# Kernel optimization log

Hardware: AMD Instinct MI355X
Metric: run time of the kernel (lower is better)

The kernel has to match this reference:

```python
import jax, jax.numpy as jnp
import numpy as np

N, E = 50000, 800000
IN, HID, HEADS, OUT = 128, 32, 4, 64
NEG_SLOPE = 0.2
BN_EPS = 1e-5


def setup_inputs() -> dict:
    key = jax.random.key(0)
    ks = jax.random.split(key, 24)
    d1 = HID * HEADS  # 128
    def glorot(k, shape):
        fan = shape[0] + shape[-1]
        return jax.random.uniform(k, shape, jnp.float32, -1.0, 1.0) * jnp.sqrt(6.0 / fan)
    inp = {
        'x': jax.random.normal(ks[0], (N, IN), jnp.float32),
        'edge_index': jax.random.randint(ks[1], (2, E), 0, N, jnp.int64),
        # layer 1: in -> hid x heads
        'W1': glorot(ks[2], (IN, d1)),
        'as1': glorot(ks[3], (HEADS, HID)),
        'ad1': glorot(ks[4], (HEADS, HID)),
        'b1': jnp.zeros((d1,), jnp.float32),
        'g1': jnp.ones((d1,), jnp.float32),
        'be1': jnp.zeros((d1,), jnp.float32),
        # layer 2: d1 -> hid x heads
        'W2': glorot(ks[5], (d1, d1)),
        'as2': glorot(ks[6], (HEADS, HID)),
        'ad2': glorot(ks[7], (HEADS, HID)),
        'b2': jnp.zeros((d1,), jnp.float32),
        'g2': jnp.ones((d1,), jnp.float32),
        'be2': jnp.zeros((d1,), jnp.float32),
        # layer 3: d1 -> out, heads=1, concat=False
        'W3': glorot(ks[8], (d1, OUT)),
        'as3': glorot(ks[9], (1, OUT)),
        'ad3': glorot(ks[10], (1, OUT)),
        'b3': jnp.zeros((OUT,), jnp.float32),
        'g3': jnp.ones((OUT,), jnp.float32),
        'be3': jnp.zeros((OUT,), jnp.float32),
    }
    return inp


def gat_conv(x, src, dst, W, a_s, a_d, b, heads, ch, concat):
    n = x.shape[0]
    h = (x @ W).reshape(n, heads, ch)                       # [N,H,C]
    al_s = jnp.sum(h * a_s, axis=-1)                        # [N,H]
    al_d = jnp.sum(h * a_d, axis=-1)                        # [N,H]
    e = jax.nn.leaky_relu(al_s[src] + al_d[dst], NEG_SLOPE)  # [E,H]
    m = jax.ops.segment_max(e, dst, num_segments=n)
    m = jnp.where(jnp.isfinite(m), m, 0.0)
    ex = jnp.exp(e - m[dst])
    denom = jax.ops.segment_sum(ex, dst, num_segments=n)
    alpha = ex / (denom[dst] + 1e-16)                       # segment softmax
    out = jax.ops.segment_sum(h[src] * alpha[:, :, None], dst, num_segments=n)
    out = out.reshape(n, heads * ch) if concat else out.mean(axis=1)
    return out + b


def batch_norm(x, g, b):
    mu = x.mean(axis=0)
    var = x.var(axis=0)
    return (x - mu) * jax.lax.rsqrt(var + BN_EPS) * g + b


def reference(x, edge_index, W1, as1, ad1, b1, g1, be1,
              W2, as2, ad2, b2, g2, be2,
              W3, as3, ad3, b3, g3, be3):
    n = x.shape[0]
    loops = jnp.arange(n, dtype=edge_index.dtype)
    src = jnp.concatenate([edge_index[0], loops])  # add_self_loops=True
    dst = jnp.concatenate([edge_index[1], loops])
    h = gat_conv(x, src, dst, W1, as1, ad1, b1, HEADS, HID, True)
    h = jax.nn.elu(batch_norm(h, g1, be1))
    h = gat_conv(h, src, dst, W2, as2, ad2, b2, HEADS, HID, True)
    h = jax.nn.elu(batch_norm(h, g2, be2))
    h = gat_conv(h, src, dst, W3, as3, ad3, b3, 1, OUT, False)
    h = jax.nn.elu(batch_norm(h, g3, be3))
    return h
```

## Files before the change

kernel.cpp:

```cpp
#include <hip/hip_runtime.h>
#include <hip/hip_bf16.h>
#include <math.h>

#define NEG_SLOPE 0.2f
#define BN_EPS 1e-5f

using short8_t = __attribute__((ext_vector_type(8))) short;
using f32x4    = __attribute__((ext_vector_type(4))) float;

__device__ __forceinline__ unsigned short f2bf(float f) {
    unsigned int u = __float_as_uint(f);
    u += 0x7FFF + ((u >> 16) & 1);
    return (unsigned short)(u >> 16);
}
__device__ __forceinline__ float bf2f(unsigned short h) {
    return __uint_as_float(((unsigned int)h) << 16);
}

__global__ void fill_i32(int* p, int v, long long n) {
    long long i = (long long)blockIdx.x * blockDim.x + threadIdx.x;
    long long st = (long long)gridDim.x * blockDim.x;
    for (; i < n; i += st) p[i] = v;
}


__global__ void dst_count(const int* __restrict__ ei, int E, int N,
                          int* __restrict__ count, int* __restrict__ ord)
{
    long long total = (long long)E + N;
    long long st = (long long)gridDim.x * blockDim.x;
    for (long long e = (long long)blockIdx.x * blockDim.x + threadIdx.x; e < total; e += st) {
        int dt = (e < E) ? ei[E + e] : (int)(e - E);
        ord[e] = atomicAdd(&count[dt], 1);
    }
}

__global__ void block_sum(const int* __restrict__ count, int* __restrict__ bsum, int N)
{
    __shared__ int sh[256];
    int b = blockIdx.x, t = threadIdx.x;
    int base = b * 1024;
    int s = 0;
    for (int i = t; i < 1024; i += 256) {
        int j = base + i;
        if (j < N) s += count[j];
    }
    sh[t] = s;
    __syncthreads();
    for (int off = 128; off > 0; off >>= 1) {
        if (t < off) sh[t] += sh[t + off];
        __syncthreads();
    }
    if (t == 0) bsum[b] = sh[0];
}

__global__ void scan_bsum(int* __restrict__ bsum, int nb, int* __restrict__ rowptr, int N, int total)
{
    __shared__ int sh[256];
    int t = threadIdx.x;
    sh[t] = (t < nb) ? bsum[t] : 0;
    __syncthreads();
    for (int off = 1; off < 256; off <<= 1) {
        int u = (t >= off) ? sh[t - off] : 0;
        __syncthreads();
        sh[t] += u;
        __syncthreads();
    }
    if (t < nb) bsum[t] = (t == 0) ? 0 : sh[t - 1];
    if (t == 0) rowptr[N] = total;
}

__global__ void scan_final(const int* __restrict__ count, const int* __restrict__ boff,
                           int* __restrict__ rowptr, int N)
{
    __shared__ int sh[256];
    int b = blockIdx.x, t = threadIdx.x;
    int base = b * 1024 + t * 4;
    int c[4];
    int s = 0;
    #pragma unroll
    for (int i = 0; i < 4; ++i) {
        int j = base + i;
        c[i] = (j < N) ? count[j] : 0;
        s += c[i];
    }
    sh[t] = s;
    __syncthreads();
    for (int off = 1; off < 256; off <<= 1) {
        int u = (t >= off) ? sh[t - off] : 0;
        __syncthreads();
        sh[t] += u;
        __syncthreads();
    }
    int run = boff[b] + ((t == 0) ? 0 : sh[t - 1]);
    #pragma unroll
    for (int i = 0; i < 4; ++i) {
        int j = base + i;
        if (j < N) rowptr[j] = run;
        run += c[i];
    }
}

__global__ void csr_scatter(const int* __restrict__ ei, int E, int N,
                            const int* __restrict__ rowptr, const int* __restrict__ ord,
                            int* __restrict__ srcs)
{
    long long total = (long long)E + N;
    long long st = (long long)gridDim.x * blockDim.x;
    for (long long e = (long long)blockIdx.x * blockDim.x + threadIdx.x; e < total; e += st) {
        int s, dt;
        if (e < E) { s = ei[e]; dt = ei[E + e]; }
        else       { s = dt = (int)(e - E); }
        srcs[rowptr[dt] + ord[e]] = s;
    }
}


template<int D>
__global__ void prep_wfrag(const float* __restrict__ W, unsigned short* __restrict__ Wf)
{
    constexpr int CS = D / 32;
    int idx = blockIdx.x * 256 + threadIdx.x;
    if (idx >= 128 * D) return;
    int i    = idx & 7;
    int lane = (idx >> 3) & 63;
    int f    = idx >> 9;
    int ks   = f & 3;
    int cs   = (f >> 2) % CS;
    int wc   = (f >> 2) / CS;
    int k = ks * 32 + ((lane >> 4) << 3) + i;
    int d = wc * (D / 2) + cs * 16 + (lane & 15);
    Wf[idx] = f2bf(W[k * D + d]);
}

template<int D, bool BN>
__global__ __launch_bounds__(256, 4) void gemm_mfma(
        const float* __restrict__ x, const unsigned short* __restrict__ Wf,
        const float* __restrict__ colstats, const float* __restrict__ g,
        const float* __restrict__ be, unsigned short* __restrict__ hbuf,
        int N, float invN)
{
    constexpr int CS = D / 32;
    __shared__ unsigned short xs[32 * 136];
    __shared__ float affA[128], affB[128];
    int tid = threadIdx.x, lane = tid & 63, w = tid >> 6;
    int wr = w >> 1, wc = w & 1;
    int n0 = blockIdx.x * 32;

    short8_t bfr[CS][4];
    #pragma unroll
    for (int cs = 0; cs < CS; ++cs)
        #pragma unroll
        for (int ks = 0; ks < 4; ++ks)
            bfr[cs][ks] = *(const short8_t*)(Wf + (((wc * CS + cs) * 4 + ks) << 9) + (lane << 3));

    if (BN) {
        if (tid < 128) {
            float cs_ = colstats[tid], cq = colstats[tid + 128];
            float mu = cs_ * invN;
            float var = cq * invN - mu * mu;
            float s = rsqrtf(var + BN_EPS) * g[tid];
            affA[tid] = s;
            affB[tid] = be[tid] - mu * s;
        }
        __syncthreads();
    }

    for (int jj = tid; jj < 32 * 32; jj += 256) {
        int r = jj >> 5, q = jj & 31;
        float4 v = make_float4(0.f, 0.f, 0.f, 0.f);
        if (n0 + r < N) v = *(const float4*)(x + (long long)(n0 + r) * 128 + q * 4);
        if (BN) {
            int c = q * 4;
            v.x = affA[c]     * v.x + affB[c];
            v.y = affA[c + 1] * v.y + affB[c + 1];
            v.z = affA[c + 2] * v.z + affB[c + 2];
            v.w = affA[c + 3] * v.w + affB[c + 3];
            v.x = (v.x > 0.f) ? v.x : expm1f(v.x);
            v.y = (v.y > 0.f) ? v.y : expm1f(v.y);
            v.z = (v.z > 0.f) ? v.z : expm1f(v.z);
            v.w = (v.w > 0.f) ? v.w : expm1f(v.w);
        }
        ushort4 o;
        o.x = f2bf(v.x); o.y = f2bf(v.y); o.z = f2bf(v.z); o.w = f2bf(v.w);
        *(ushort4*)(xs + r * 136 + q * 4) = o;
    }
    __syncthreads();

    f32x4 acc[CS];
    #pragma unroll
    for (int cs = 0; cs < CS; ++cs) acc[cs] = (f32x4){0.f, 0.f, 0.f, 0.f};

    #pragma unroll
    for (int ks = 0; ks < 4; ++ks) {
        short8_t a = *(const short8_t*)(xs + (wr * 16 + (lane & 15)) * 136
                                           + ks * 32 + ((lane >> 4) << 3));
        #pragma unroll
        for (int cs = 0; cs < CS; ++cs)
            acc[cs] = __builtin_amdgcn_mfma_f32_16x16x32_bf16(a, bfr[cs][ks], acc[cs], 0, 0, 0);
    }

    int mrow = wr * 16 + ((lane >> 4) << 2);
    int dcol = wc * (D / 2) + (lane & 15);
    #pragma unroll
    for (int cs = 0; cs < CS; ++cs)
        #pragma unroll
        for (int r = 0; r < 4; ++r) {
            int n = n0 + mrow + r;
            if (n < N) hbuf[(long long)n * D + dcol + cs * 16] = f2bf(acc[cs][r]);
        }
}

template<int H, int C>
__global__ void calc_al(const unsigned short* __restrict__ hbuf,
                        const float* __restrict__ a_s, const float* __restrict__ a_d,
                        float* __restrict__ als, float* __restrict__ ald, int N)
{
    int idx = blockIdx.x * blockDim.x + threadIdx.x;
    if (idx >= N * H) return;
    int n = idx / H, hh = idx % H;
    const unsigned short* hp = hbuf + (long long)n * H * C + hh * C;
    float s1 = 0.f, s2 = 0.f;
    #pragma unroll
    for (int c = 0; c < C; c += 4) {
        ushort4 hv = *(const ushort4*)(hp + c);
        float f0 = bf2f(hv.x), f1 = bf2f(hv.y), f2 = bf2f(hv.z), f3 = bf2f(hv.w);
        s1 += f0 * a_s[hh * C + c]     + f1 * a_s[hh * C + c + 1]
            + f2 * a_s[hh * C + c + 2] + f3 * a_s[hh * C + c + 3];
        s2 += f0 * a_d[hh * C + c]     + f1 * a_d[hh * C + c + 1]
            + f2 * a_d[hh * C + c + 2] + f3 * a_d[hh * C + c + 3];
    }
    als[idx] = s1;
    ald[idx] = s2;
}

template<int H, int C>
__global__ __launch_bounds__(256) void gat_aggregate_v5(
        const int* __restrict__ rowptr, const int* __restrict__ srcs,
        const float* __restrict__ als, const float* __restrict__ ald,
        const unsigned short* __restrict__ hbuf, float* __restrict__ agg,
        float* __restrict__ part, int N)
{
    constexpr int D = H * C;
    constexpr int TPN = D / 8;
    constexpr int NPB = 256 / TPN;
    __shared__ float red[4][TPN * 16];
    int tid = threadIdx.x;
    int g = tid / TPN, l = tid % TPN;
    int n = blockIdx.x * NPB + g;
    bool active = (n < N);
    int c0 = l * 8;
    int hh = c0 / C;
    float aldv = active ? ald[(long long)n * H + hh] : 0.f;
    int beg = 0, end = 0;
    if (active) { beg = rowptr[n]; end = rowptr[n + 1]; }

    float wsum = 0.f;
    float acc[8];
    #pragma unroll
    for (int i = 0; i < 8; ++i) acc[i] = 0.f;

    int e = beg;
    for (; e + 4 <= end; e += 4) {
        int s0 = srcs[e], s1 = srcs[e + 1], s2 = srcs[e + 2], s3 = srcs[e + 3];
        float v0 = als[(long long)s0 * H + hh] + aldv;
        float v1 = als[(long long)s1 * H + hh] + aldv;
        float v2 = als[(long long)s2 * H + hh] + aldv;
        float v3 = als[(long long)s3 * H + hh] + aldv;
        v0 = (v0 >= 0.f) ? v0 : NEG_SLOPE * v0;
        v1 = (v1 >= 0.f) ? v1 : NEG_SLOPE * v1;
        v2 = (v2 >= 0.f) ? v2 : NEG_SLOPE * v2;
        v3 = (v3 >= 0.f) ? v3 : NEG_SLOPE * v3;
        float w0 = __expf(v0), w1 = __expf(v1), w2 = __expf(v2), w3 = __expf(v3);
        float4 q0 = *(const float4*)(hbuf + (long long)s0 * D + c0);
        float4 q1 = *(const float4*)(hbuf + (long long)s1 * D + c0);
        float4 q2 = *(const float4*)(hbuf + (long long)s2 * D + c0);
        float4 q3 = *(const float4*)(hbuf + (long long)s3 * D + c0);
        wsum += w0 + w1 + w2 + w3;
        const float* qf0 = (const float*)&q0;
        const float* qf1 = (const float*)&q1;
        const float* qf2 = (const float*)&q2;
        const float* qf3 = (const float*)&q3;
        #pragma unroll
        for (int i = 0; i < 4; ++i) {
            unsigned int u0 = __float_as_uint(qf0[i]);
            unsigned int u1 = __float_as_uint(qf1[i]);
            unsigned int u2 = __float_as_uint(qf2[i]);
            unsigned int u3 = __float_as_uint(qf3[i]);
            acc[2*i]   += w0 * __uint_as_float(u0 << 16)
                        + w1 * __uint_as_float(u1 << 16)
                        + w2 * __uint_as_float(u2 << 16)
                        + w3 * __uint_as_float(u3 << 16);
            acc[2*i+1] += w0 * __uint_as_float(u0 & 0xFFFF0000u)
                        + w1 * __uint_as_float(u1 & 0xFFFF0000u)
                        + w2 * __uint_as_float(u2 & 0xFFFF0000u)
                        + w3 * __uint_as_float(u3 & 0xFFFF0000u);
        }
    }
    for (; e < end; ++e) {
        int s = srcs[e];
        float v = als[(long long)s * H + hh] + aldv;
        v = (v >= 0.f) ? v : NEG_SLOPE * v;
        float w = __expf(v);
        float4 q = *(const float4*)(hbuf + (long long)s * D + c0);
        const float* qf = (const float*)&q;
        wsum += w;
        #pragma unroll
        for (int i = 0; i < 4; ++i) {
            unsigned int u = __float_as_uint(qf[i]);
            acc[2*i]   += w * __uint_as_float(u << 16);
            acc[2*i+1] += w * __uint_as_float(u & 0xFFFF0000u);
        }
    }
    float inv = active ? 1.f / (wsum + 1e-16f) : 0.f;
    float sv[16];
    #pragma unroll
    for (int i = 0; i < 8; ++i) {
        float o = acc[i] * inv;
        sv[i] = o;
        sv[8 + i] = o * o;
        acc[i] = o;
    }
    if (active) {
        *(float4*)(agg + (long long)n * D + c0)     = make_float4(acc[0], acc[1], acc[2], acc[3]);
        *(float4*)(agg + (long long)n * D + c0 + 4) = make_float4(acc[4], acc[5], acc[6], acc[7]);
    }

    #pragma unroll
    for (int off = TPN; off < 64; off <<= 1)
        #pragma unroll
        for (int j = 0; j < 16; ++j)
            sv[j] += __shfl_xor(sv[j], off);

    int w4 = tid >> 6, lane = tid & 63;
    if (lane < TPN) {
        #pragma unroll
        for (int j = 0; j < 16; ++j) red[w4][lane * 16 + j] = sv[j];
    }
    __syncthreads();
    if (w4 == 0 && lane < TPN) {
        #pragma unroll
        for (int ww = 1; ww < 4; ++ww)
            #pragma unroll
            for (int j = 0; j < 16; ++j) sv[j] += red[ww][lane * 16 + j];
        float* p = part + (long long)blockIdx.x * (2 * D) + lane * 16;
        *(float4*)(p)      = make_float4(sv[0],  sv[1],  sv[2],  sv[3]);
        *(float4*)(p + 4)  = make_float4(sv[4],  sv[5],  sv[6],  sv[7]);
        *(float4*)(p + 8)  = make_float4(sv[8],  sv[9],  sv[10], sv[11]);
        *(float4*)(p + 12) = make_float4(sv[12], sv[13], sv[14], sv[15]);
    }
}

template<int D>
__global__ __launch_bounds__(256) void reduce_stats(
        const float* __restrict__ part, int nblk, float* __restrict__ colsum)
{
    __shared__ float sh[256];
    int f = blockIdx.x;
    int t = threadIdx.x;
    int col = (f < D) ? f : (f - D);
    int off = (col / 8) * 16 + (col % 8) + ((f < D) ? 0 : 8);
    float s = 0.f;
    for (int i = t; i < nblk; i += 256)
        s += part[(long long)i * (2 * D) + off];
    sh[t] = s;
    __syncthreads();
    for (int o = 128; o > 0; o >>= 1) {
        if (t < o) sh[t] += sh[t + o];
        __syncthreads();
    }
    if (t == 0) colsum[(f < D) ? f : (128 + f - D)] = sh[0];
}

template<int D>
__global__ __launch_bounds__(256) void bn_apply_v2(
        const float* __restrict__ agg, const float* __restrict__ colsum,
        const float* __restrict__ g, const float* __restrict__ be,
        float* __restrict__ out, int N, float invN)
{
    constexpr int TPR = D / 4;
    constexpr int RPB = 256 / TPR;
    __shared__ float affA[D], affB[D];
    int tid = threadIdx.x;
    if (tid < D) {
        float mu = colsum[tid] * invN;
        float var = colsum[128 + tid] * invN - mu * mu;
        float s = rsqrtf(var + BN_EPS) * g[tid];
        affA[tid] = s;
        affB[tid] = be[tid] - mu * s;
    }
    __syncthreads();
    int rg = tid / TPR, cl = tid % TPR;
    int c = cl * 4;
    float a0 = affA[c], a1 = affA[c+1], a2 = affA[c+2], a3 = affA[c+3];
    float b0 = affB[c], b1 = affB[c+1], b2 = affB[c+2], b3 = affB[c+3];
    for (int r = blockIdx.x * RPB + rg; r < N; r += gridDim.x * RPB) {
        float4 v = *(const float4*)(agg + (long long)r * D + c);
        v.x = a0 * v.x + b0; v.y = a1 * v.y + b1;
        v.z = a2 * v.z + b2; v.w = a3 * v.w + b3;
        v.x = (v.x > 0.f) ? v.x : expm1f(v.x);
        v.y = (v.y > 0.f) ? v.y : expm1f(v.y);
        v.z = (v.z > 0.f) ? v.z : expm1f(v.z);
        v.w = (v.w > 0.f) ? v.w : expm1f(v.w);
        *(float4*)(out + (long long)r * D + c) = v;
    }
}

template<int H, int C, bool BN>
static void run_layer(const float* xin, int N,
                      const int* rowptr, const int* srcs,
                      const unsigned short* Wf, const float* a_s, const float* a_d,
                      const float* prev_stats, const float* prev_g, const float* prev_be,
                      unsigned short* hbuf, float* als, float* ald,
                      float* part, float* stats_out, float* agg,
                      hipStream_t stream)
{
    constexpr int D = H * C;
    constexpr int NPB = 256 / (D / 8);
    int nblk = (N + NPB - 1) / NPB;
    float invN = 1.f / (float)N;
    gemm_mfma<D, BN><<<(N + 31) / 32, 256, 0, stream>>>(
        xin, Wf, prev_stats, prev_g, prev_be, hbuf, N, invN);
    calc_al<H, C><<<(N * H + 255) / 256, 256, 0, stream>>>(hbuf, a_s, a_d, als, ald, N);
    gat_aggregate_v5<H, C><<<nblk, 256, 0, stream>>>(
        rowptr, srcs, als, ald, hbuf, agg, part, N);
    reduce_stats<D><<<2 * D, 256, 0, stream>>>(part, nblk, stats_out);
}

extern "C" void kernel_launch(void* const* d_in, const int* in_sizes, int n_in,
                              void* d_out, int out_size, void* d_ws, size_t ws_size,
                              hipStream_t stream)
{
    const float* x   = (const float*)d_in[0];
    const int*   ei  = (const int*)d_in[1];
    const float* W1  = (const float*)d_in[2];
    const float* as1 = (const float*)d_in[3];
    const float* ad1 = (const float*)d_in[4];
    const float* g1  = (const float*)d_in[6];
    const float* be1 = (const float*)d_in[7];
    const float* W2  = (const float*)d_in[8];
    const float* as2 = (const float*)d_in[9];
    const float* ad2 = (const float*)d_in[10];
    const float* g2  = (const float*)d_in[12];
    const float* be2 = (const float*)d_in[13];
    const float* W3  = (const float*)d_in[14];
    const float* as3 = (const float*)d_in[15];
    const float* ad3 = (const float*)d_in[16];
    const float* g3  = (const float*)d_in[18];
    const float* be3 = (const float*)d_in[19];

    const int N = in_sizes[0] / 128;
    const int E = in_sizes[1] / 2;
    const int NB = (N + 1023) / 1024;
    const int NBLK128 = (N + 15) / 16;

    float* ws   = (float*)d_ws;
    float* aggA = ws;
    float* aggB = aggA + (long long)N * 128;
    float* als  = aggB + (long long)N * 128;
    float* ald  = als  + (long long)N * 4;
    float* cs0  = ald  + (long long)N * 4;
    float* cs1  = cs0 + 256;
    float* cs2  = cs1 + 256;
    unsigned short* hbuf = (unsigned short*)(cs2 + 256);
    int*   rowptr = (int*)(hbuf + (long long)N * 128);
    int*   count  = rowptr + (N + 1);
    int*   bsum   = count + N;
    int*   ord    = bsum + 256;
    int*   srcs   = ord + ((long long)E + N);
    unsigned short* wf1 = (unsigned short*)(srcs + ((long long)E + N));
    unsigned short* wf2 = wf1 + 128 * 128;
    unsigned short* wf3 = wf2 + 128 * 128;
    float* part = (float*)(wf3 + 128 * 64);

    prep_wfrag<128><<<64, 256, 0, stream>>>(W1, wf1);
    prep_wfrag<128><<<64, 256, 0, stream>>>(W2, wf2);
    prep_wfrag<64><<<32, 256, 0, stream>>>(W3, wf3);

    fill_i32<<<128, 256, 0, stream>>>(count, 0, N);
    dst_count<<<2048, 256, 0, stream>>>(ei, E, N, count, ord);
    block_sum<<<NB, 256, 0, stream>>>(count, bsum, N);
    scan_bsum<<<1, 256, 0, stream>>>(bsum, NB, rowptr, N, E + N);
    scan_final<<<NB, 256, 0, stream>>>(count, bsum, rowptr, N);
    csr_scatter<<<2048, 256, 0, stream>>>(ei, E, N, rowptr, ord, srcs);

    run_layer<4, 32, false>(x, N, rowptr, srcs, wf1, as1, ad1,
                            nullptr, nullptr, nullptr,
                            hbuf, als, ald, part, cs0, aggA, stream);
    run_layer<4, 32, true>(aggA, N, rowptr, srcs, wf2, as2, ad2,
                           cs0, g1, be1,
                           hbuf, als, ald, part, cs1, aggB, stream);
    run_layer<1, 64, true>(aggB, N, rowptr, srcs, wf3, as3, ad3,
                           cs1, g2, be2,
                           hbuf, als, ald, part, cs2, aggA, stream);
    bn_apply_v2<64><<<2048, 256, 0, stream>>>(aggA, cs2, g3, be3, (float*)d_out, N, 1.f / (float)N);
}
```

Before: 247.6 us.

## Fuse attention logit computation into GEMM epilogue and merge setup kernels

Computes the per-node source and destination attention scores inside the MFMA GEMM epilogue, using register accumulators, lane shuffles and a small shared-memory reduction for the single-head layer. This removes the separate calc_al kernel and its re-read of hbuf. Separately, the three weight-fragment prep kernels and the count zero-fill are merged into one setup kernel to cut launch count. The scores now come from fp32 accumulators instead of bf16-rounded h, which changes numerics slightly. The epilogue also adds register pressure and a block barrier to the GEMM.

```diff
diff --git a/kernel.cpp b/kernel.cpp
--- a/kernel.cpp
+++ b/kernel.cpp
@@ -17,111 +17,12 @@
     return __uint_as_float(((unsigned int)h) << 16);
 }
 
-__global__ void fill_i32(int* p, int v, long long n) {
-    long long i = (long long)blockIdx.x * blockDim.x + threadIdx.x;
-    long long st = (long long)gridDim.x * blockDim.x;
-    for (; i < n; i += st) p[i] = v;
-}
-
-
-__global__ void dst_count(const int* __restrict__ ei, int E, int N,
-                          int* __restrict__ count, int* __restrict__ ord)
-{
-    long long total = (long long)E + N;
-    long long st = (long long)gridDim.x * blockDim.x;
-    for (long long e = (long long)blockIdx.x * blockDim.x + threadIdx.x; e < total; e += st) {
-        int dt = (e < E) ? ei[E + e] : (int)(e - E);
-        ord[e] = atomicAdd(&count[dt], 1);
-    }
-}
-
-__global__ void block_sum(const int* __restrict__ count, int* __restrict__ bsum, int N)
-{
-    __shared__ int sh[256];
-    int b = blockIdx.x, t = threadIdx.x;
-    int base = b * 1024;
-    int s = 0;
-    for (int i = t; i < 1024; i += 256) {
-        int j = base + i;
-        if (j < N) s += count[j];
-    }
-    sh[t] = s;
-    __syncthreads();
-    for (int off = 128; off > 0; off >>= 1) {
-        if (t < off) sh[t] += sh[t + off];
-        __syncthreads();
-    }
-    if (t == 0) bsum[b] = sh[0];
-}
-
-__global__ void scan_bsum(int* __restrict__ bsum, int nb, int* __restrict__ rowptr, int N, int total)
-{
-    __shared__ int sh[256];
-    int t = threadIdx.x;
-    sh[t] = (t < nb) ? bsum[t] : 0;
-    __syncthreads();
-    for (int off = 1; off < 256; off <<= 1) {
-        int u = (t >= off) ? sh[t - off] : 0;
-        __syncthreads();
-        sh[t] += u;
-        __syncthreads();
-    }
-    if (t < nb) bsum[t] = (t == 0) ? 0 : sh[t - 1];
-    if (t == 0) rowptr[N] = total;
-}
-
-__global__ void scan_final(const int* __restrict__ count, const int* __restrict__ boff,
-                           int* __restrict__ rowptr, int N)
-{
-    __shared__ int sh[256];
-    int b = blockIdx.x, t = threadIdx.x;
-    int base = b * 1024 + t * 4;
-    int c[4];
-    int s = 0;
-    #pragma unroll
-    for (int i = 0; i < 4; ++i) {
-        int j = base + i;
-        c[i] = (j < N) ? count[j] : 0;
-        s += c[i];
-    }
-    sh[t] = s;
-    __syncthreads();
-    for (int off = 1; off < 256; off <<= 1) {
-        int u = (t >= off) ? sh[t - off] : 0;
-        __syncthreads();
-        sh[t] += u;
-        __syncthreads();
-    }
-    int run = boff[b] + ((t == 0) ? 0 : sh[t - 1]);
-    #pragma unroll
-    for (int i = 0; i < 4; ++i) {
-        int j = base + i;
-        if (j < N) rowptr[j] = run;
-        run += c[i];
-    }
-}
-
-__global__ void csr_scatter(const int* __restrict__ ei, int E, int N,
-                            const int* __restrict__ rowptr, const int* __restrict__ ord,
-                            int* __restrict__ srcs)
-{
-    long long total = (long long)E + N;
-    long long st = (long long)gridDim.x * blockDim.x;
-    for (long long e = (long long)blockIdx.x * blockDim.x + threadIdx.x; e < total; e += st) {
-        int s, dt;
-        if (e < E) { s = ei[e]; dt = ei[E + e]; }
-        else       { s = dt = (int)(e - E); }
-        srcs[rowptr[dt] + ord[e]] = s;
-    }
-}
-
-
-template<int D>
-__global__ void prep_wfrag(const float* __restrict__ W, unsigned short* __restrict__ Wf)
-{
-    constexpr int CS = D / 32;
-    int idx = blockIdx.x * 256 + threadIdx.x;
-    if (idx >= 128 * D) return;
+
+__device__ __forceinline__ void wfrag_one(const float* __restrict__ W,
+                                          unsigned short* __restrict__ Wf,
+                                          int idx, int D)
+{
+    int CS = D / 32;
     int i    = idx & 7;
     int lane = (idx >> 3) & 63;
     int f    = idx >> 9;
@@ -133,16 +34,129 @@
     Wf[idx] = f2bf(W[k * D + d]);
 }
 
-template<int D, bool BN>
+__global__ void setup_all(const float* __restrict__ W1, const float* __restrict__ W2,
+                          const float* __restrict__ W3,
+                          unsigned short* __restrict__ wf1, unsigned short* __restrict__ wf2,
+                          unsigned short* __restrict__ wf3,
+                          int* __restrict__ count, int N)
+{
+    int total = 16384 + 16384 + 8192 + N;
+    int st = gridDim.x * blockDim.x;
+    for (int idx = blockIdx.x * blockDim.x + threadIdx.x; idx < total; idx += st) {
+        if (idx < 16384)       wfrag_one(W1, wf1, idx, 128);
+        else if (idx < 32768)  wfrag_one(W2, wf2, idx - 16384, 128);
+        else if (idx < 40960)  wfrag_one(W3, wf3, idx - 32768, 64);
+        else                   count[idx - 40960] = 0;
+    }
+}
+
+
+__global__ void dst_count(const int* __restrict__ ei, int E, int N,
+                          int* __restrict__ count, int* __restrict__ ord)
+{
+    long long total = (long long)E + N;
+    long long st = (long long)gridDim.x * blockDim.x;
+    for (long long e = (long long)blockIdx.x * blockDim.x + threadIdx.x; e < total; e += st) {
+        int dt = (e < E) ? ei[E + e] : (int)(e - E);
+        ord[e] = atomicAdd(&count[dt], 1);
+    }
+}
+
+__global__ void block_sum(const int* __restrict__ count, int* __restrict__ bsum, int N)
+{
+    __shared__ int sh[256];
+    int b = blockIdx.x, t = threadIdx.x;
+    int base = b * 1024;
+    int s = 0;
+    for (int i = t; i < 1024; i += 256) {
+        int j = base + i;
+        if (j < N) s += count[j];
+    }
+    sh[t] = s;
+    __syncthreads();
+    for (int off = 128; off > 0; off >>= 1) {
+        if (t < off) sh[t] += sh[t + off];
+        __syncthreads();
+    }
+    if (t == 0) bsum[b] = sh[0];
+}
+
+__global__ void scan_bsum(int* __restrict__ bsum, int nb, int* __restrict__ rowptr, int N, int total)
+{
+    __shared__ int sh[256];
+    int t = threadIdx.x;
+    sh[t] = (t < nb) ? bsum[t] : 0;
+    __syncthreads();
+    for (int off = 1; off < 256; off <<= 1) {
+        int u = (t >= off) ? sh[t - off] : 0;
+        __syncthreads();
+        sh[t] += u;
+        __syncthreads();
+    }
+    if (t < nb) bsum[t] = (t == 0) ? 0 : sh[t - 1];
+    if (t == 0) rowptr[N] = total;
+}
+
+__global__ void scan_final(const int* __restrict__ count, const int* __restrict__ boff,
+                           int* __restrict__ rowptr, int N)
+{
+    __shared__ int sh[256];
+    int b = blockIdx.x, t = threadIdx.x;
+    int base = b * 1024 + t * 4;
+    int c[4];
+    int s = 0;
+    #pragma unroll
+    for (int i = 0; i < 4; ++i) {
+        int j = base + i;
+        c[i] = (j < N) ? count[j] : 0;
+        s += c[i];
+    }
+    sh[t] = s;
+    __syncthreads();
+    for (int off = 1; off < 256; off <<= 1) {
+        int u = (t >= off) ? sh[t - off] : 0;
+        __syncthreads();
+        sh[t] += u;
+        __syncthreads();
+    }
+    int run = boff[b] + ((t == 0) ? 0 : sh[t - 1]);
+    #pragma unroll
+    for (int i = 0; i < 4; ++i) {
+        int j = base + i;
+        if (j < N) rowptr[j] = run;
+        run += c[i];
+    }
+}
+
+__global__ void csr_scatter(const int* __restrict__ ei, int E, int N,
+                            const int* __restrict__ rowptr, const int* __restrict__ ord,
+                            int* __restrict__ srcs)
+{
+    long long total = (long long)E + N;
+    long long st = (long long)gridDim.x * blockDim.x;
+    for (long long e = (long long)blockIdx.x * blockDim.x + threadIdx.x; e < total; e += st) {
+        int s, dt;
+        if (e < E) { s = ei[e]; dt = ei[E + e]; }
+        else       { s = dt = (int)(e - E); }
+        srcs[rowptr[dt] + ord[e]] = s;
+    }
+}
+
+
+template<int D, int H, bool BN>
 __global__ __launch_bounds__(256, 4) void gemm_mfma(
         const float* __restrict__ x, const unsigned short* __restrict__ Wf,
         const float* __restrict__ colstats, const float* __restrict__ g,
-        const float* __restrict__ be, unsigned short* __restrict__ hbuf,
+        const float* __restrict__ be,
+        const float* __restrict__ a_s, const float* __restrict__ a_d,
+        unsigned short* __restrict__ hbuf,
+        float* __restrict__ als, float* __restrict__ ald,
         int N, float invN)
 {
     constexpr int CS = D / 32;
     __shared__ unsigned short xs[32 * 136];
     __shared__ float affA[128], affB[128];
+    __shared__ float red2[4][4][4][2];
     int tid = threadIdx.x, lane = tid & 63, w = tid >> 6;
     int wr = w >> 1, wc = w & 1;
     int n0 = blockIdx.x * 32;
@@ -209,29 +223,88 @@
             int n = n0 + mrow + r;
             if (n < N) hbuf[(long long)n * D + dcol + cs * 16] = f2bf(acc[cs][r]);
         }
-}
-
-template<int H, int C>
-__global__ void calc_al(const unsigned short* __restrict__ hbuf,
-                        const float* __restrict__ a_s, const float* __restrict__ a_d,
-                        float* __restrict__ als, float* __restrict__ ald, int N)
-{
-    int idx = blockIdx.x * blockDim.x + threadIdx.x;
-    if (idx >= N * H) return;
-    int n = idx / H, hh = idx % H;
-    const unsigned short* hp = hbuf + (long long)n * H * C + hh * C;
-    float s1 = 0.f, s2 = 0.f;
-    #pragma unroll
-    for (int c = 0; c < C; c += 4) {
-        ushort4 hv = *(const ushort4*)(hp + c);
-        float f0 = bf2f(hv.x), f1 = bf2f(hv.y), f2 = bf2f(hv.z), f3 = bf2f(hv.w);
-        s1 += f0 * a_s[hh * C + c]     + f1 * a_s[hh * C + c + 1]
-            + f2 * a_s[hh * C + c + 2] + f3 * a_s[hh * C + c + 3];
-        s2 += f0 * a_d[hh * C + c]     + f1 * a_d[hh * C + c + 1]
-            + f2 * a_d[hh * C + c + 2] + f3 * a_d[hh * C + c + 3];
-    }
-    als[idx] = s1;
-    ald[idx] = s2;
+
+    int l15 = lane & 15;
+    if (H == 4) {
+        float ps[2][4], pd[2][4];
+        #pragma unroll
+        for (int ch = 0; ch < 2; ++ch) {
+            int hh = wc * 2 + ch;
+            #pragma unroll
+            for (int r = 0; r < 4; ++r) { ps[ch][r] = 0.f; pd[ch][r] = 0.f; }
+            #pragma unroll
+            for (int k2 = 0; k2 < 2; ++k2) {
+                int cs = ch * 2 + k2;
+                int cih = k2 * 16 + l15;
+                float as_v = a_s[hh * 32 + cih];
+                float ad_v = a_d[hh * 32 + cih];
+                #pragma unroll
+                for (int r = 0; r < 4; ++r) {
+                    ps[ch][r] += acc[cs][r] * as_v;
+                    pd[ch][r] += acc[cs][r] * ad_v;
+                }
+            }
+        }
+        #pragma unroll
+        for (int off = 1; off < 16; off <<= 1)
+            #pragma unroll
+            for (int ch = 0; ch < 2; ++ch)
+                #pragma unroll
+                for (int r = 0; r < 4; ++r) {
+                    ps[ch][r] += __shfl_xor(ps[ch][r], off);
+                    pd[ch][r] += __shfl_xor(pd[ch][r], off);
+                }
+        if (l15 == 0) {
+            #pragma unroll
+            for (int r = 0; r < 4; ++r) {
+                int n = n0 + mrow + r;
+                if (n < N) {
+                    #pragma unroll
+                    for (int ch = 0; ch < 2; ++ch) {
+                        als[(long long)n * 4 + wc * 2 + ch] = ps[ch][r];
+                        ald[(long long)n * 4 + wc * 2 + ch] = pd[ch][r];
+                    }
+                }
+            }
+        }
+    } else {
+        float ps[4], pd[4];
+        #pragma unroll
+        for (int r = 0; r < 4; ++r) { ps[r] = 0.f; pd[r] = 0.f; }
+        #pragma unroll
+        for (int cs = 0; cs < CS; ++cs) {
+            int c = wc * 32 + cs * 16 + l15;
+            float as_v = a_s[c], ad_v = a_d[c];
+            #pragma unroll
+            for (int r = 0; r < 4; ++r) {
+                ps[r] += acc[cs][r] * as_v;
+                pd[r] += acc[cs][r] * ad_v;
+            }
+        }
+        #pragma unroll
+        for (int off = 1; off < 16; off <<= 1)
+            #pragma unroll
+            for (int r = 0; r < 4; ++r) {
+                ps[r] += __shfl_xor(ps[r], off);
+                pd[r] += __shfl_xor(pd[r], off);
+            }
+        int q = lane >> 4;
+        if (l15 == 0) {
+            #pragma unroll
+            for (int r = 0; r < 4; ++r) {
+                red2[w][q][r][0] = ps[r];
+                red2[w][q][r][1] = pd[r];
+            }
+        }
+        __syncthreads();
+        if (tid < 64) {
+            int wr2 = tid >> 5, row = (tid >> 1) & 15, sd = tid & 1;
+            int qq = row >> 2, rr = row & 3;
+            float v = red2[wr2 * 2][qq][rr][sd] + red2[wr2 * 2 + 1][qq][rr][sd];
+            int n = n0 + wr2 * 16 + row;
+            if (n < N) { if (sd) ald[n] = v; else als[n] = v; }
+        }
+    }
 }
 
 template<int H, int C>
@@ -419,9 +492,8 @@
     constexpr int NPB = 256 / (D / 8);
     int nblk = (N + NPB - 1) / NPB;
     float invN = 1.f / (float)N;
-    gemm_mfma<D, BN><<<(N + 31) / 32, 256, 0, stream>>>(
-        xin, Wf, prev_stats, prev_g, prev_be, hbuf, N, invN);
-    calc_al<H, C><<<(N * H + 255) / 256, 256, 0, stream>>>(hbuf, a_s, a_d, als, ald, N);
+    gemm_mfma<D, H, BN><<<(N + 31) / 32, 256, 0, stream>>>(
+        xin, Wf, prev_stats, prev_g, prev_be, a_s, a_d, hbuf, als, ald, N, invN);
     gat_aggregate_v5<H, C><<<nblk, 256, 0, stream>>>(
         rowptr, srcs, als, ald, hbuf, agg, part, N);
     reduce_stats<D><<<2 * D, 256, 0, stream>>>(part, nblk, stats_out);
@@ -452,7 +524,6 @@
     const int N = in_sizes[0] / 128;
     const int E = in_sizes[1] / 2;
     const int NB = (N + 1023) / 1024;
-    const int NBLK128 = (N + 15) / 16;
 
     float* ws   = (float*)d_ws;
     float* aggA = ws;
@@ -473,11 +544,8 @@
     unsigned short* wf3 = wf2 + 128 * 128;
     float* part = (float*)(wf3 + 128 * 64);
 
-    prep_wfrag<128><<<64, 256, 0, stream>>>(W1, wf1);
-    prep_wfrag<128><<<64, 256, 0, stream>>>(W2, wf2);
-    prep_wfrag<64><<<32, 256, 0, stream>>>(W3, wf3);
-
-    fill_i32<<<128, 256, 0, stream>>>(count, 0, N);
+    setup_all<<<356, 256, 0, stream>>>(W1, W2, W3, wf1, wf2, wf3, count, N);
+
     dst_count<<<2048, 256, 0, stream>>>(ei, E, N, count, ord);
     block_sum<<<NB, 256, 0, stream>>>(count, bsum, N);
     scan_bsum<<<1, 256, 0, stream>>>(bsum, NB, rowptr, N, E + N);
```

New measurement: 227.3 us (median of 2 runs). 1.09x faster.
